# Kernel tuning notes

Hardware: AMD Instinct MI355X
Metric: run time of the kernel (lower is better)

The kernel has to match this reference:

```python
import jax, jax.numpy as jnp
import numpy as np

EPS = 1e-5

def _bn(x):
    # BatchNorm (training-mode batch stats, gamma=1, beta=0) over batch+spatial axes
    axes = (0,) + tuple(range(2, x.ndim))
    m = x.mean(axis=axes, keepdims=True)
    v = x.var(axis=axes, keepdims=True)
    return (x - m) / jnp.sqrt(v + EPS)

def _knn(x, k):
    # x: [B, C, N] -> idx [B, N, K] of k nearest neighbors (largest of negative sq dist)
    xt = jnp.swapaxes(x, 1, 2)                      # [B, N, C]
    inner = -2.0 * jnp.einsum('bnc,bmc->bnm', xt, xt)
    xx = jnp.sum(x * x, axis=1)                     # [B, N]
    pdist = -xx[:, :, None] - inner - xx[:, None, :]  # [B, N, N] (negative sq dist)
    return jax.lax.top_k(pdist, k)[1]

def _get_neighbors(x, k):
    # x: [B, C, N] -> edge features [B, 2C, N, K] = concat(neighbor - center, center)
    idx = _knn(x, k)                                # [B, N, K]
    xt = jnp.swapaxes(x, 1, 2)                      # [B, N, C]
    nb = jax.vmap(lambda pts, i: pts[i])(xt, idx)   # [B, N, K, C]
    center = jnp.broadcast_to(xt[:, :, None, :], nb.shape)
    feat = jnp.concatenate([nb - center, center], axis=-1)  # [B, N, K, 2C]
    return jnp.transpose(feat, (0, 3, 1, 2))        # [B, 2C, N, K]

def _sa_layer(x, Wq, Wk, Wt, bt):
    # Faithful SALayerSingleHead: note original computes x_v but never uses it,
    # and uses x @ attention; we match that math exactly. x: [B, C, N]
    xq = jnp.einsum('qc,bcn->bnq', Wq, x)           # [B, N, C/4]
    xk = jnp.einsum('qc,bcn->bqn', Wk, x)           # [B, C/4, N]
    energy = jnp.einsum('bnq,bqm->bnm', xq, xk)     # [B, N, N]
    attn = jax.nn.softmax(energy, axis=-1)
    attn = attn / (1e-6 + attn.sum(axis=1, keepdims=True))
    xr = jnp.einsum('bcn,bnm->bcm', x, attn)        # [B, C, N]
    xr = jax.nn.relu(_bn(jnp.einsum('oc,bcn->bon', Wt, x - xr) + bt[None, :, None]))
    return x + xr

def setup_inputs() -> dict:
    key = jax.random.key(0)
    ks = jax.random.split(key, 12)
    B, N, K = 8, 2048, 32
    s = 0.02
    inp = {
        'x': jax.random.normal(ks[0], (B, 3, N), dtype=jnp.float32),
        'We1': jax.random.normal(ks[1], (64, 6), dtype=jnp.float32) * s,
        'be1': jnp.zeros((64,), jnp.float32),
        'We2': jax.random.normal(ks[2], (64, 128), dtype=jnp.float32) * s,
        'be2': jnp.zeros((64,), jnp.float32),
        'Wq': jax.random.normal(ks[3], (4, 32, 128), dtype=jnp.float32) * s,
        'Wk': jax.random.normal(ks[4], (4, 32, 128), dtype=jnp.float32) * s,
        'Wt': jax.random.normal(ks[5], (4, 128, 128), dtype=jnp.float32) * s,
        'bt': jnp.zeros((4, 128), jnp.float32),
        'Wf': jax.random.normal(ks[6], (1024, 512), dtype=jnp.float32) * s,
        'bf': jnp.zeros((1024,), jnp.float32),
        'Wc1': jax.random.normal(ks[7], (512, 1536), dtype=jnp.float32) * s,
        'bc1': jnp.zeros((512,), jnp.float32),
        'Wc2': jax.random.normal(ks[8], (256, 512), dtype=jnp.float32) * s,
        'bc2': jnp.zeros((256,), jnp.float32),
        'Wc3': jax.random.normal(ks[9], (13, 256), dtype=jnp.float32) * s,
        'bc3': jnp.zeros((13,), jnp.float32),
        'k': K,
    }
    return inp

def reference(x, We1, be1, We2, be2, Wq, Wk, Wt, bt, Wf, bf, Wc1, bc1, Wc2, bc2, Wc3, bc3, k):
    # EdgeConv block 1: xyz -> 64
    e1 = jnp.einsum('oc,bcnk->bonk', We1, _get_neighbors(x, k)) + be1[None, :, None, None]
    f1 = jax.nn.relu(_bn(e1)).max(axis=-1)          # [B, 64, N]
    # EdgeConv block 2: 64 -> 64
    e2 = jnp.einsum('oc,bcnk->bonk', We2, _get_neighbors(f1, k)) + be2[None, :, None, None]
    f2 = jax.nn.relu(_bn(e2)).max(axis=-1)          # [B, 64, N]
    feat = jnp.concatenate([f1, f2], axis=1)        # [B, 128, N]
    # 4 stacked single-head SA layers (PCT offset attention)
    xs = feat
    outs = []
    for i in range(4):
        xs = _sa_layer(xs, Wq[i], Wk[i], Wt[i], bt[i])
        outs.append(xs)
    cat = jnp.concatenate(outs, axis=1)             # [B, 512, N]
    fuse = jax.nn.relu(_bn(jnp.einsum('oc,bcn->bon', Wf, cat) + bf[None, :, None]))  # [B,1024,N]
    g = fuse.max(axis=-1)                           # [B, 1024]
    gl = jnp.broadcast_to(g[:, :, None], (g.shape[0], g.shape[1], cat.shape[2]))
    h = jnp.concatenate([gl, cat], axis=1)          # [B, 1536, N]
    h = jax.nn.relu(_bn(jnp.einsum('oc,bcn->bon', Wc1, h) + bc1[None, :, None]))
    h = jax.nn.relu(_bn(jnp.einsum('oc,bcn->bon', Wc2, h) + bc2[None, :, None]))
    out = jnp.einsum('oc,bcn->bon', Wc3, h) + bc3[None, :, None]  # [B, 13, N]
    return out
```

## Files before the change

### kernel.cpp

```cpp
#include <hip/hip_runtime.h>
#include <math.h>

#define DEV static __device__ __forceinline__

namespace {

constexpr int B = 8;
constexpr int N = 2048;
constexpr int KNN = 32;
constexpr float BNEPS = 1e-5f;

DEV unsigned f2key(float f) {
  unsigned u = __float_as_uint(f);
  return (u & 0x80000000u) ? ~u : (u | 0x80000000u);
}

DEV void atomicMaxFloat(float* addr, float val) {
  if (val >= 0.0f) atomicMax((int*)addr, __float_as_int(val));
  else atomicMin((unsigned int*)addr, (unsigned int)__float_as_int(val));
}

struct SelScratch {
  unsigned hist[256];
  int ss[257];
  int bin;
  int cnt;
};

template <int NK>
DEV unsigned long long radix_select32(const unsigned long long (&keys)[NK], SelScratch& s) {
  const int t = threadIdx.x;
  const int lane = t & 63, wave = t >> 6;
  unsigned long long prefix = 0; unsigned long long T = 0;
  int needed = KNN;
  bool done = false;
  for (int level = 0; level < 8 && !done; ++level) {
    int shift = 56 - 8 * level;
    s.hist[t] = 0;
    __syncthreads();
    unsigned long long maskhi = level ? (~0ull << (64 - 8 * level)) : 0ull;
    #pragma unroll
    for (int j = 0; j < NK; ++j) {
      if ((keys[j] & maskhi) == prefix)
        atomicAdd(&s.hist[(unsigned)(keys[j] >> shift) & 255u], 1u);
    }
    __syncthreads();
    if (wave == 0) {
      unsigned h0 = s.hist[4 * lane], h1 = s.hist[4 * lane + 1], h2 = s.hist[4 * lane + 2], h3 = s.hist[4 * lane + 3];
      unsigned s3 = h3, s2 = h2 + s3, s1 = h1 + s2, s0 = h0 + s1;
      unsigned suf = s0;
      #pragma unroll
      for (int off = 1; off < 64; off <<= 1) {
        unsigned v = __shfl_down(suf, off);
        if (lane + off < 64) suf += v;
      }
      unsigned above = suf - s0;
      s.ss[4 * lane] = (int)(s0 + above); s.ss[4 * lane + 1] = (int)(s1 + above);
      s.ss[4 * lane + 2] = (int)(s2 + above); s.ss[4 * lane + 3] = (int)(s3 + above);
      if (lane == 63) s.ss[256] = 0;
    }
    __syncthreads();
    if (s.ss[t] >= needed && s.ss[t + 1] < needed) s.bin = t;
    __syncthreads();
    int bin = s.bin;
    int hc = (int)s.hist[bin];
    needed -= s.ss[bin + 1];
    prefix |= ((unsigned long long)(unsigned)bin) << shift;
    if (needed == hc) { T = prefix; done = true; }
    __syncthreads();
  }
  return T;
}

template <int NK>
DEV void collect32(const unsigned long long (&keys)[NK], unsigned long long T, SelScratch& s,
                   int* __restrict__ out) {
  if (threadIdx.x == 0) s.cnt = 0;
  __syncthreads();
  #pragma unroll
  for (int j = 0; j < NK; ++j) {
    if (keys[j] >= T) {
      int pos = atomicAdd(&s.cnt, 1);
      out[pos] = (int)~(unsigned)keys[j];
    }
  }
  __syncthreads();
}

__global__ __launch_bounds__(256) void knn1_kernel(const float* __restrict__ x, int* __restrict__ idx) {
  __shared__ SelScratch s;
  __shared__ double cc[3];
  int bn = blockIdx.x, b = bn >> 11, n = bn & (N - 1);
  int t = threadIdx.x;
  const float* xb = x + (size_t)b * 3 * N;
  if (t < 3) cc[t] = (double)xb[(size_t)t * N + n];
  __syncthreads();
  double cx = cc[0], cy = cc[1], cz = cc[2];
  unsigned long long keys[8];
  #pragma unroll
  for (int j = 0; j < 8; ++j) {
    int m = t + 256 * j;
    double dx = (double)xb[m] - cx, dy = (double)xb[N + m] - cy, dz = (double)xb[2 * N + m] - cz;
    double pd = -(dx * dx + dy * dy + dz * dz);
    keys[j] = ((unsigned long long)f2key((float)pd) << 32) | (unsigned)~m;
  }
  __syncthreads();
  unsigned long long T = radix_select32(keys, s);
  collect32(keys, T, s, idx + (size_t)bn * KNN);
}

__global__ __launch_bounds__(256) void edge1_kernel(const float* __restrict__ x, const int* __restrict__ idx,
    const float* __restrict__ We1, const float* __restrict__ be1,
    float* __restrict__ emax, double* __restrict__ epart) {
  __shared__ float Ws[6][65];
  __shared__ float fs[6][33];
  __shared__ float es[64][33];
  __shared__ int  is[KNN];
  int bn = blockIdx.x, b = bn >> 11, n = bn & (N - 1);
  int t = threadIdx.x;
  if (t < KNN) is[t] = idx[(size_t)bn * KNN + t];
  for (int e = t; e < 64 * 6; e += 256) Ws[e % 6][e / 6] = We1[e];
  __syncthreads();
  const float* xb = x + (size_t)b * 3 * N;
  for (int e = t; e < 6 * KNN; e += 256) {
    int c = e >> 5, k = e & 31;
    int m = is[k];
    fs[c][k] = (c < 3) ? (xb[(size_t)c * N + m] - xb[(size_t)c * N + n]) : xb[(size_t)(c - 3) * N + n];
  }
  __syncthreads();
  int k = t & 31, orow = t >> 5;
  float acc[8];
  #pragma unroll
  for (int j = 0; j < 8; ++j) acc[j] = 0.0f;
  #pragma unroll
  for (int c = 0; c < 6; ++c) {
    float fv = fs[c][k];
    #pragma unroll
    for (int j = 0; j < 8; ++j) acc[j] = __fadd_rn(acc[j], __fmul_rn(Ws[c][orow * 8 + j], fv));
  }
  #pragma unroll
  for (int j = 0; j < 8; ++j) es[orow * 8 + j][k] = __fadd_rn(acc[j], be1[orow * 8 + j]);
  __syncthreads();
  if (t < 64) {
    double sum = 0, s2 = 0; float mx = -3.402823466e38f;
    #pragma unroll 8
    for (int kk = 0; kk < KNN; ++kk) {
      float v = es[t][kk]; double dv = (double)v;
      sum += dv; s2 = fma(dv, dv, s2); mx = fmaxf(mx, v);
    }
    emax[((size_t)b * 64 + t) * N + n] = mx;
    epart[(size_t)bn * 128 + t] = sum;
    epart[(size_t)bn * 128 + 64 + t] = s2;
  }
}

__global__ __launch_bounds__(256) void edge_stats_kernel(const double* __restrict__ epart, float* __restrict__ ems) {
  __shared__ double r1[256], r2[256];
  int o = blockIdx.x, t = threadIdx.x;
  double s = 0, s2 = 0;
  for (int i = t; i < B * N; i += 256) { s += epart[(size_t)i * 128 + o]; s2 += epart[(size_t)i * 128 + 64 + o]; }
  r1[t] = s; r2[t] = s2; __syncthreads();
  for (int st = 128; st > 0; st >>= 1) { if (t < st) { r1[t] += r1[t + st]; r2[t] += r2[t + st]; } __syncthreads(); }
  if (t == 0) {
    double cnt = (double)(B * N * KNN);
    double m = r1[0] / cnt, v = r2[0] / cnt - m * m;
    ems[o] = (float)m; ems[64 + o] = (float)v;
  }
}

__global__ __launch_bounds__(256) void edge_finish_kernel(const float* __restrict__ emax, const float* __restrict__ ems,
                                                          float* __restrict__ f) {
  size_t i = (size_t)blockIdx.x * 256 + threadIdx.x;
  int c = (int)((i >> 11) & 63);
  float sd = sqrtf(ems[64 + c] + BNEPS);
  float v = (emax[i] - ems[c]) / sd;
  f[i] = v > 0.f ? v : 0.f;
}

__global__ __launch_bounds__(256) void transpose_f1_kernel(const float* __restrict__ f1, float* __restrict__ f1t) {
  size_t i = (size_t)blockIdx.x * 256 + threadIdx.x;
  int n = (int)(i & (N - 1)); int c = (int)((i >> 11) & 63); int b = (int)(i >> 17);
  f1t[((size_t)b * N + n) * 64 + c] = f1[i];
}

__global__ __launch_bounds__(256) void xx2_kernel(const float* __restrict__ f1, double* __restrict__ xx2) {
  int i = blockIdx.x * 256 + threadIdx.x;
  int b = i >> 11, n = i & (N - 1);
  const float* p = f1 + (size_t)b * 64 * N + n;
  double s = 0;
  #pragma unroll 16
  for (int c = 0; c < 64; ++c) { double v = (double)p[(size_t)c * N]; s = fma(v, v, s); }
  xx2[i] = s;
}

__global__ __launch_bounds__(256) void knn2_kernel(const float* __restrict__ f1, const float* __restrict__ f1t,
                                                   const double* __restrict__ xx2, int* __restrict__ idx) {
  __shared__ SelScratch s;
  __shared__ double ctr[4][64];
  int bx = blockIdx.x, b = bx >> 9, n0 = (bx & 511) * 4;
  int t = threadIdx.x;
  { int i = t >> 6, c = t & 63; ctr[i][c] = (double)f1t[((size_t)b * N + n0 + i) * 64 + c]; }
  __syncthreads();
  const float* fb = f1 + (size_t)b * 64 * N;
  const double* xxb = xx2 + (size_t)b * N;
  double xxn0 = xxb[n0], xxn1 = xxb[n0 + 1], xxn2 = xxb[n0 + 2], xxn3 = xxb[n0 + 3];
  unsigned long long keys[4][8];
  #pragma unroll 1
  for (int j = 0; j < 8; ++j) {
    int m = t + 256 * j;
    double a0 = 0, a1 = 0, a2 = 0, a3 = 0;
    #pragma unroll 8
    for (int c = 0; c < 64; ++c) {
      double v = (double)fb[(size_t)c * N + m];
      a0 = fma(v, ctr[0][c], a0); a1 = fma(v, ctr[1][c], a1);
      a2 = fma(v, ctr[2][c], a2); a3 = fma(v, ctr[3][c], a3);
    }
    double xxm = xxb[m];
    double p0 = -xxn0 + 2.0 * a0 - xxm, p1 = -xxn1 + 2.0 * a1 - xxm;
    double p2 = -xxn2 + 2.0 * a2 - xxm, p3 = -xxn3 + 2.0 * a3 - xxm;
    unsigned long long lo = (unsigned)~m;
    keys[0][j] = ((unsigned long long)f2key((float)p0) << 32) | lo;
    keys[1][j] = ((unsigned long long)f2key((float)p1) << 32) | lo;
    keys[2][j] = ((unsigned long long)f2key((float)p2) << 32) | lo;
    keys[3][j] = ((unsigned long long)f2key((float)p3) << 32) | lo;
  }
  __syncthreads();
  #pragma unroll 1
  for (int i = 0; i < 4; ++i) {
    unsigned long long T = radix_select32(keys[i], s);
    collect32(keys[i], T, s, idx + ((size_t)b * N + n0 + i) * KNN);
  }
}

__global__ __launch_bounds__(256) void edge2_kernel(const float* __restrict__ f1t, const int* __restrict__ idx,
    const float* __restrict__ We2, const float* __restrict__ be2,
    float* __restrict__ emax, double* __restrict__ epart) {
  __shared__ float smem[8448];
  __shared__ int is[4][32];
  float (*Ws)[65] = (float(*)[65])smem;
  float* fsb = smem + 2080;
  int bx = blockIdx.x;
  int b = bx >> 9, n0 = (bx & 511) * 4;
  int t = threadIdx.x;
  if (t < 128) is[t >> 5][t & 31] = idx[((size_t)b * N + n0 + (t >> 5)) * KNN + (t & 31)];
  int k = t & 31, p = (t >> 5) & 3, oh = t >> 7;
  float acc[32];
  #pragma unroll
  for (int j = 0; j < 32; ++j) acc[j] = 0.f;
  const float* fbt = f1t + (size_t)b * N * 64;
  for (int cc = 0; cc < 4; ++cc) {
    int c0 = cc * 32;
    __syncthreads();
    for (int e = t; e < 2048; e += 256) Ws[e & 31][e >> 5] = We2[(size_t)(e >> 5) * 128 + c0 + (e & 31)];
    for (int e = t; e < 4096; e += 256) {
      int c = e & 31, kk = (e >> 5) & 31, pp = e >> 10;
      int m = is[pp][kk];
      int cg = c0 + c;
      float v = (cg < 64) ? (fbt[(size_t)m * 64 + cg] - fbt[(size_t)(n0 + pp) * 64 + cg])
                          : fbt[(size_t)(n0 + pp) * 64 + (cg - 64)];
      fsb[(pp * 32 + c) * 33 + kk] = v;
    }
    __syncthreads();
    #pragma unroll 4
    for (int c = 0; c < 32; ++c) {
      float fv = fsb[(p * 32 + c) * 33 + k];
      #pragma unroll
      for (int j = 0; j < 32; ++j) acc[j] = fmaf(Ws[c][oh * 32 + j], fv, acc[j]);
    }
  }
  __syncthreads();
  #pragma unroll
  for (int j = 0; j < 32; ++j) smem[((p * 64 + oh * 32 + j)) * 33 + k] = acc[j] + be2[oh * 32 + j];
  __syncthreads();
  {
    int pp = t >> 6, o = t & 63;
    const float* ep = smem + (pp * 64 + o) * 33;
    double sum = 0, s2 = 0; float mx = -3.402823466e38f;
    #pragma unroll 8
    for (int kk = 0; kk < KNN; ++kk) {
      float v = ep[kk]; double dv = (double)v;
      sum += dv; s2 = fma(dv, dv, s2); mx = fmaxf(mx, v);
    }
    int n = n0 + pp;
    emax[((size_t)b * 64 + o) * N + n] = mx;
    epart[((size_t)b * N + n) * 128 + o] = sum;
    epart[((size_t)b * N + n) * 128 + 64 + o] = s2;
  }
}

__global__ __launch_bounds__(256) void concat_feat_kernel(const float* __restrict__ f1, const float* __restrict__ f2,
                                                          float* __restrict__ feat) {
  size_t i = (size_t)blockIdx.x * 256 + threadIdx.x;
  int n = (int)(i & (N - 1)); int c = (int)((i >> 11) & 127); int b = (int)(i >> 18);
  feat[i] = (c < 64) ? f1[((size_t)b * 64 + c) * N + n] : f2[((size_t)b * 64 + (c - 64)) * N + n];
}

__global__ __launch_bounds__(256) void sa_qk_kernel(const float* __restrict__ xs, int xs_bstride, int xs_coff,
    const float* __restrict__ Wq, const float* __restrict__ Wk,
    float* __restrict__ xq, float* __restrict__ xk) {
  __shared__ __align__(16) float Ws[32][68];
  __shared__ __align__(16) float vs[32][68];
  int bx = blockIdx.x, b = bx >> 5, n0 = (bx & 31) * 64;
  int t = threadIdx.x;
  int tc = t >> 4, tm = t & 15;
  float acc[4][4];
  #pragma unroll
  for (int i = 0; i < 4; ++i)
    #pragma unroll
    for (int j = 0; j < 4; ++j) acc[i][j] = 0.f;
  for (int cc = 0; cc < 4; ++cc) {
    int c0 = cc * 32;
    __syncthreads();
    for (int e = t; e < 512; e += 256) {
      int o = e >> 3, cq = e & 7;
      float4 w4 = (o < 32) ? *(const float4*)&Wq[o * 128 + c0 + cq * 4]
                           : *(const float4*)&Wk[(o - 32) * 128 + c0 + cq * 4];
      Ws[cq * 4 + 0][o] = w4.x; Ws[cq * 4 + 1][o] = w4.y; Ws[cq * 4 + 2][o] = w4.z; Ws[cq * 4 + 3][o] = w4.w;
    }
    for (int e = t; e < 512; e += 256) {
      int c = e >> 4, nq = e & 15;
      *(float4*)&vs[c][nq * 4] =
          *(const float4*)&xs[(size_t)b * xs_bstride + (size_t)(xs_coff + c0 + c) * N + n0 + nq * 4];
    }
    __syncthreads();
    #pragma unroll 4
    for (int c = 0; c < 32; ++c) {
      float4 w4 = *(const float4*)&Ws[c][tc * 4];
      float4 v4 = *(const float4*)&vs[c][tm * 4];
      float wv[4] = {w4.x, w4.y, w4.z, w4.w};
      float vv[4] = {v4.x, v4.y, v4.z, v4.w};
      #pragma unroll
      for (int i = 0; i < 4; ++i)
        #pragma unroll
        for (int j = 0; j < 4; ++j) acc[i][j] = fmaf(wv[i], vv[j], acc[i][j]);
    }
  }
  #pragma unroll
  for (int i = 0; i < 4; ++i) {
    int o2 = tc * 4 + i;
    if (o2 < 32) {
      #pragma unroll
      for (int j = 0; j < 4; ++j) {
        int n = n0 + tm * 4 + j;
        xq[((size_t)b * N + n) * 32 + o2] = acc[i][j];
      }
    } else {
      float4 o4 = make_float4(acc[i][0], acc[i][1], acc[i][2], acc[i][3]);
      *(float4*)&xk[((size_t)b * 32 + (o2 - 32)) * N + n0 + tm * 4] = o4;
    }
  }
}

__global__ __launch_bounds__(256) void sa_rowstats_kernel(const float* __restrict__ xq, const float* __restrict__ xk,
    float* __restrict__ rowmax, float* __restrict__ rowsum) {
  __shared__ float qs[16][33];
  __shared__ float wred[4][16][2];
  int bx = blockIdx.x;
  int b = bx >> 7, n0 = (bx & 127) * 16;
  int t = threadIdx.x;
  for (int e = t; e < 16 * 32; e += 256) qs[e >> 5][e & 31] = xq[((size_t)b * N + n0 + (e >> 5)) * 32 + (e & 31)];
  __syncthreads();
  float rm[16], rs[16];
  #pragma unroll
  for (int r = 0; r < 16; ++r) { rm[r] = -3.402823466e38f; rs[r] = 0.f; }
  const float* xkb = xk + (size_t)b * 32 * N;
  for (int m = t; m < N; m += 256) {
    float kv[32];
    #pragma unroll
    for (int q = 0; q < 32; ++q) kv[q] = xkb[(size_t)q * N + m];
    #pragma unroll 4
    for (int r = 0; r < 16; ++r) {
      float e = 0;
      #pragma unroll
      for (int q = 0; q < 32; ++q) e = fmaf(qs[r][q], kv[q], e);
      if (e > rm[r]) { rs[r] = rs[r] * __expf(rm[r] - e) + 1.0f; rm[r] = e; }
      else rs[r] += __expf(e - rm[r]);
    }
  }
  int lane = t & 63, w = t >> 6;
  #pragma unroll 1
  for (int r = 0; r < 16; ++r) {
    float m1 = rm[r], s1 = rs[r];
    #pragma unroll
    for (int off = 32; off > 0; off >>= 1) {
      float m2 = __shfl_xor(m1, off), s2 = __shfl_xor(s1, off);
      float mm = fmaxf(m1, m2);
      s1 = s1 * __expf(m1 - mm) + s2 * __expf(m2 - mm);
      m1 = mm;
    }
    if (lane == 0) { wred[w][r][0] = m1; wred[w][r][1] = s1; }
  }
  __syncthreads();
  if (t < 16) {
    float M = wred[0][t][0], S = wred[0][t][1];
    #pragma unroll
    for (int w2 = 1; w2 < 4; ++w2) {
      float m2 = wred[w2][t][0], s2 = wred[w2][t][1];
      float mm = fmaxf(M, m2);
      S = S * __expf(M - mm) + s2 * __expf(m2 - mm);
      M = mm;
    }
    rowmax[(size_t)b * N + n0 + t] = M;
    rowsum[(size_t)b * N + n0 + t] = S;
  }
}

__global__ __launch_bounds__(256) void sa_attny_kernel(const float* __restrict__ xs, int xs_bstride, int xs_coff,
    const float* __restrict__ xq, const float* __restrict__ xk,
    const float* __restrict__ rowmax, const float* __restrict__ rowsum,
    float* __restrict__ Yp, float* __restrict__ cspart) {
  __shared__ __align__(16) float qs[64][36];
  __shared__ float rmv[64], rsv[64];
  __shared__ __align__(16) float Ps[64][68];
  __shared__ __align__(16) float vs[64][132];
  __shared__ float csr[4][64];
  int bx = blockIdx.x;
  int g = bx & 3, m0 = ((bx >> 2) & 31) * 64, b = bx >> 7;
  int t = threadIdx.x;
  int tc = t >> 4, tm = t & 15;
  int tmm = t & 63, tns = t >> 6;
  float kreg[32];
  #pragma unroll
  for (int q = 0; q < 32; ++q) kreg[q] = xk[((size_t)b * 32 + q) * N + m0 + tmm];
  float acc[2][4][4];
  #pragma unroll
  for (int h = 0; h < 2; ++h)
    #pragma unroll
    for (int i = 0; i < 4; ++i)
      #pragma unroll
      for (int j = 0; j < 4; ++j) acc[h][i][j] = 0.f;
  float cs = 0.f;
  const float* xsb = xs + (size_t)b * xs_bstride + (size_t)xs_coff * N;
  for (int nt = g * 8; nt < g * 8 + 8; ++nt) {
    int n0 = nt * 64;
    __syncthreads();
    for (int e = t; e < 512; e += 256) {
      int nn = e >> 3, qq = e & 7;
      *(float4*)&qs[nn][qq * 4] = *(const float4*)&xq[((size_t)b * N + n0 + nn) * 32 + qq * 4];
    }
    if (t < 64) { rmv[t] = rowmax[(size_t)b * N + n0 + t]; rsv[t] = 1.0f / rowsum[(size_t)b * N + n0 + t]; }
    for (int e = t; e < 128 * 64; e += 256) { int c = e >> 6, nn = e & 63; vs[nn][c] = xsb[(size_t)c * N + n0 + nn]; }
    __syncthreads();
    float cp = 0.f;
    #pragma unroll 1
    for (int jj = 0; jj < 16; ++jj) {
      int nn = tns * 16 + jj;
      float ea = 0, eb = 0, ec = 0, ed = 0;
      #pragma unroll
      for (int q4 = 0; q4 < 8; ++q4) {
        float4 qv = *(const float4*)&qs[nn][q4 * 4];
        ea = fmaf(qv.x, kreg[4 * q4 + 0], ea);
        eb = fmaf(qv.y, kreg[4 * q4 + 1], eb);
        ec = fmaf(qv.z, kreg[4 * q4 + 2], ec);
        ed = fmaf(qv.w, kreg[4 * q4 + 3], ed);
      }
      float e2 = (ea + eb) + (ec + ed);
      float p = __expf(e2 - rmv[nn]) * rsv[nn];
      Ps[nn][tmm] = p; cp += p;
    }
    csr[tns][tmm] = cp;
    __syncthreads();
    if (t < 64) cs += csr[0][t] + csr[1][t] + csr[2][t] + csr[3][t];
    #pragma unroll 2
    for (int nn = 0; nn < 64; ++nn) {
      float4 pa = *(const float4*)&Ps[nn][tm * 4];
      float4 x0 = *(const float4*)&vs[nn][tc * 4];
      float4 x1 = *(const float4*)&vs[nn][64 + tc * 4];
      float pvv[4] = {pa.x, pa.y, pa.z, pa.w};
      float xv0[4] = {x0.x, x0.y, x0.z, x0.w};
      float xv1[4] = {x1.x, x1.y, x1.z, x1.w};
      #pragma unroll
      for (int i = 0; i < 4; ++i)
        #pragma unroll
        for (int jm = 0; jm < 4; ++jm) {
          acc[0][i][jm] = fmaf(xv0[i], pvv[jm], acc[0][i][jm]);
          acc[1][i][jm] = fmaf(xv1[i], pvv[jm], acc[1][i][jm]);
        }
    }
  }
  #pragma unroll
  for (int h = 0; h < 2; ++h)
    #pragma unroll
    for (int i = 0; i < 4; ++i) {
      float4 o4 = make_float4(acc[h][i][0], acc[h][i][1], acc[h][i][2], acc[h][i][3]);
      *(float4*)&Yp[(((size_t)g * B + b) * 128 + h * 64 + tc * 4 + i) * N + m0 + tm * 4] = o4;
    }
  if (t < 64) cspart[((size_t)g * B + b) * N + m0 + t] = cs;
}

__global__ __launch_bounds__(256) void sa_wt_kernel(const float* __restrict__ xs, int xs_bstride, int xs_coff,
    const float* __restrict__ Yp, const float* __restrict__ cspart,
    const float* __restrict__ Wt, const float* __restrict__ bt,
    float* __restrict__ tpre) {
  __shared__ __align__(16) float Ws[32][132];
  __shared__ __align__(16) float vs[32][68];
  __shared__ __align__(16) float inv[64];
  int bx = blockIdx.x, b = bx >> 5, n0 = (bx & 31) * 64;
  int t = threadIdx.x;
  if (t < 64) {
    float s = 0;
    #pragma unroll
    for (int g = 0; g < 4; ++g) s += cspart[((size_t)g * B + b) * N + n0 + t];
    inv[t] = 1.0f / (1e-6f + s);
  }
  int tc = t >> 4, tm = t & 15;
  float acc[8][4];
  #pragma unroll
  for (int jc = 0; jc < 8; ++jc)
    #pragma unroll
    for (int jm = 0; jm < 4; ++jm) acc[jc][jm] = 0.f;
  for (int cc = 0; cc < 4; ++cc) {
    int c0 = cc * 32;
    __syncthreads();
    for (int e = t; e < 1024; e += 256) {
      int o = e >> 3, cq = e & 7;
      float4 w4 = *(const float4*)&Wt[o * 128 + c0 + cq * 4];
      Ws[cq * 4 + 0][o] = w4.x; Ws[cq * 4 + 1][o] = w4.y; Ws[cq * 4 + 2][o] = w4.z; Ws[cq * 4 + 3][o] = w4.w;
    }
    for (int e = t; e < 512; e += 256) {
      int c = e >> 4, nq = e & 15;
      float4 xv = *(const float4*)&xs[(size_t)b * xs_bstride + (size_t)(xs_coff + c0 + c) * N + n0 + nq * 4];
      float4 ys = make_float4(0.f, 0.f, 0.f, 0.f);
      #pragma unroll
      for (int g = 0; g < 4; ++g) {
        float4 yv = *(const float4*)&Yp[(((size_t)g * B + b) * 128 + c0 + c) * N + n0 + nq * 4];
        ys.x += yv.x; ys.y += yv.y; ys.z += yv.z; ys.w += yv.w;
      }
      float4 iv = *(const float4*)&inv[nq * 4];
      float4 r = make_float4(xv.x - ys.x * iv.x, xv.y - ys.y * iv.y, xv.z - ys.z * iv.z, xv.w - ys.w * iv.w);
      *(float4*)&vs[c][nq * 4] = r;
    }
    __syncthreads();
    #pragma unroll 4
    for (int c = 0; c < 32; ++c) {
      float4 w0 = *(const float4*)&Ws[c][tc * 4];
      float4 w1 = *(const float4*)&Ws[c][tc * 4 + 64];
      float4 v4 = *(const float4*)&vs[c][tm * 4];
      float wv[8] = {w0.x, w0.y, w0.z, w0.w, w1.x, w1.y, w1.z, w1.w};
      float vv[4] = {v4.x, v4.y, v4.z, v4.w};
      #pragma unroll
      for (int jc = 0; jc < 8; ++jc)
        #pragma unroll
        for (int jm = 0; jm < 4; ++jm) acc[jc][jm] = fmaf(wv[jc], vv[jm], acc[jc][jm]);
    }
  }
  #pragma unroll
  for (int jc = 0; jc < 8; ++jc) {
    int o2 = tc * 4 + (jc & 3) + (jc >> 2) * 64;
    float bias = bt[o2];
    float4 o4 = make_float4(acc[jc][0] + bias, acc[jc][1] + bias, acc[jc][2] + bias, acc[jc][3] + bias);
    *(float4*)&tpre[((size_t)b * 128 + o2) * N + n0 + tm * 4] = o4;
  }
}

__global__ __launch_bounds__(256) void chanstats_kernel(const float* __restrict__ x, float* __restrict__ ms, int C) {
  __shared__ double r1[256], r2[256];
  int c = blockIdx.x, t = threadIdx.x;
  double s = 0, s2 = 0;
  for (int i = t; i < B * N; i += 256) {
    int b = i >> 11, n = i & (N - 1);
    double v = (double)x[((size_t)b * C + c) * N + n];
    s += v; s2 = fma(v, v, s2);
  }
  r1[t] = s; r2[t] = s2; __syncthreads();
  for (int st = 128; st > 0; st >>= 1) { if (t < st) { r1[t] += r1[t + st]; r2[t] += r2[t + st]; } __syncthreads(); }
  if (t == 0) {
    double cnt = (double)(B * N);
    double m = r1[0] / cnt, v = r2[0] / cnt - m * m;
    ms[c] = (float)m; ms[C + c] = (float)v;
  }
}

__global__ __launch_bounds__(256) void sa_out_kernel(const float* __restrict__ tpre, const float* __restrict__ ms,
    const float* __restrict__ xs, int xs_bstride, int xs_coff, float* __restrict__ cat, int lay) {
  size_t i = (size_t)blockIdx.x * 256 + threadIdx.x;
  int n = (int)(i & (N - 1)); int c = (int)((i >> 11) & 127); int b = (int)(i >> 18);
  float sd = sqrtf(ms[128 + c] + BNEPS);
  float v = (tpre[i] - ms[c]) / sd;
  v = v > 0.f ? v : 0.f;
  float xv = xs[(size_t)b * xs_bstride + (size_t)(xs_coff + c) * N + n];
  cat[((size_t)b * 512 + lay * 128 + c) * N + n] = xv + v;
}

__global__ __launch_bounds__(256) void fuse_kernel(const float* __restrict__ cat, const float* __restrict__ Wf,
    const float* __restrict__ bf, float* __restrict__ fps, float* __restrict__ fps2, float* __restrict__ premax) {
  __shared__ __align__(16) float smem[8320];
  float (*Ws)[132] = (float(*)[132])smem;
  float (*vs)[68] = (float(*)[68])(smem + 4224);
  int bx = blockIdx.x;
  int b = bx >> 8, o0 = ((bx >> 5) & 7) * 128, n0 = (bx & 31) * 64;
  int part = b * 32 + (bx & 31);
  int t = threadIdx.x, tc = t >> 4, tm = t & 15;
  float acc[8][4];
  #pragma unroll
  for (int jc = 0; jc < 8; ++jc)
    #pragma unroll
    for (int jm = 0; jm < 4; ++jm) acc[jc][jm] = 0.f;
  for (int cc = 0; cc < 16; ++cc) {
    int c0 = cc * 32;
    __syncthreads();
    for (int e = t; e < 1024; e += 256) {
      int o = e >> 3, cq = e & 7;
      float4 w4 = *(const float4*)&Wf[(size_t)(o0 + o) * 512 + c0 + cq * 4];
      Ws[cq * 4 + 0][o] = w4.x; Ws[cq * 4 + 1][o] = w4.y; Ws[cq * 4 + 2][o] = w4.z; Ws[cq * 4 + 3][o] = w4.w;
    }
    for (int e = t; e < 512; e += 256) {
      int c = e >> 4, nq = e & 15;
      *(float4*)&vs[c][nq * 4] = *(const float4*)&cat[((size_t)b * 512 + c0 + c) * N + n0 + nq * 4];
    }
    __syncthreads();
    #pragma unroll 4
    for (int c = 0; c < 32; ++c) {
      float4 w0 = *(const float4*)&Ws[c][tc * 4];
      float4 w1 = *(const float4*)&Ws[c][tc * 4 + 64];
      float4 v4 = *(const float4*)&vs[c][tm * 4];
      float wv[8] = {w0.x, w0.y, w0.z, w0.w, w1.x, w1.y, w1.z, w1.w};
      float vv[4] = {v4.x, v4.y, v4.z, v4.w};
      #pragma unroll
      for (int jc = 0; jc < 8; ++jc)
        #pragma unroll
        for (int jm = 0; jm < 4; ++jm) acc[jc][jm] = fmaf(wv[jc], vv[jm], acc[jc][jm]);
    }
  }
  __syncthreads();
  #pragma unroll
  for (int jc = 0; jc < 8; ++jc) {
    int o = tc * 4 + (jc & 3) + (jc >> 2) * 64;
    float bias = bf[o0 + o];
    #pragma unroll
    for (int jm = 0; jm < 4; ++jm) smem[o * 65 + tm * 4 + jm] = acc[jc][jm] + bias;
  }
  __syncthreads();
  if (t < 128) {
    double s = 0, s2 = 0; float mx = -3.402823466e38f;
    const float* dp = smem + t * 65;
    #pragma unroll 8
    for (int nn = 0; nn < 64; ++nn) {
      float v = dp[nn]; double dv = (double)v;
      s += dv; s2 = fma(dv, dv, s2); mx = fmaxf(mx, v);
    }
    fps[(size_t)(o0 + t) * 256 + part] = (float)s;
    fps2[(size_t)(o0 + t) * 256 + part] = (float)s2;
    atomicMaxFloat(&premax[(size_t)b * 1024 + o0 + t], mx);
  }
}

__global__ __launch_bounds__(256) void fuse_stats_kernel(const float* __restrict__ fps, const float* __restrict__ fps2,
                                                         float* __restrict__ ms) {
  __shared__ double r1[256], r2[256];
  int o = blockIdx.x, t = threadIdx.x;
  r1[t] = (double)fps[(size_t)o * 256 + t];
  r2[t] = (double)fps2[(size_t)o * 256 + t];
  __syncthreads();
  for (int st = 128; st > 0; st >>= 1) { if (t < st) { r1[t] += r1[t + st]; r2[t] += r2[t + st]; } __syncthreads(); }
  if (t == 0) {
    double cnt = (double)(B * N);
    double m = r1[0] / cnt, v = r2[0] / cnt - m * m;
    ms[o] = (float)m; ms[1024 + o] = (float)v;
  }
}

__global__ void g_kernel(const float* __restrict__ premax, const float* __restrict__ ms, float* __restrict__ g) {
  int i = blockIdx.x * 256 + threadIdx.x;
  int o = i & 1023;
  float sd = sqrtf(ms[1024 + o] + BNEPS);
  float v = (premax[i] - ms[o]) / sd;
  g[i] = v > 0.f ? v : 0.f;
}

__global__ __launch_bounds__(256) void gproj_kernel(const float* __restrict__ Wc1, const float* __restrict__ g,
                                                    float* __restrict__ gproj) {
  int i = blockIdx.x * 256 + threadIdx.x;
  int b = i >> 9, o = i & 511;
  const float* gb = g + (size_t)b * 1024;
  const float* wr = Wc1 + (size_t)o * 1536;
  float s = 0;
  #pragma unroll 8
  for (int c = 0; c < 1024; ++c) s = fmaf(wr[c], gb[c], s);
  gproj[i] = s;
}

__global__ __launch_bounds__(256) void mlp_gemm_kernel(const float* __restrict__ in, int Cin,
    const float* __restrict__ W, int wstride, int wcoff,
    const float* __restrict__ bias, const float* __restrict__ extra, int Cout,
    float* __restrict__ out) {
  __shared__ __align__(16) float Ws[32][132];
  __shared__ __align__(16) float vs[32][68];
  int otiles = Cout >> 7;
  int bx = blockIdx.x;
  int b = bx / (otiles * 32); int rem = bx % (otiles * 32);
  int o0 = (rem >> 5) * 128, n0 = (rem & 31) * 64;
  int t = threadIdx.x, tc = t >> 4, tm = t & 15;
  float acc[8][4];
  #pragma unroll
  for (int jc = 0; jc < 8; ++jc)
    #pragma unroll
    for (int jm = 0; jm < 4; ++jm) acc[jc][jm] = 0.f;
  for (int c0 = 0; c0 < Cin; c0 += 32) {
    __syncthreads();
    for (int e = t; e < 1024; e += 256) {
      int o = e >> 3, cq = e & 7;
      float4 w4 = *(const float4*)&W[(size_t)(o0 + o) * wstride + wcoff + c0 + cq * 4];
      Ws[cq * 4 + 0][o] = w4.x; Ws[cq * 4 + 1][o] = w4.y; Ws[cq * 4 + 2][o] = w4.z; Ws[cq * 4 + 3][o] = w4.w;
    }
    for (int e = t; e < 512; e += 256) {
      int c = e >> 4, nq = e & 15;
      *(float4*)&vs[c][nq * 4] = *(const float4*)&in[((size_t)b * Cin + c0 + c) * N + n0 + nq * 4];
    }
    __syncthreads();
    #pragma unroll 4
    for (int c = 0; c < 32; ++c) {
      float4 w0 = *(const float4*)&Ws[c][tc * 4];
      float4 w1 = *(const float4*)&Ws[c][tc * 4 + 64];
      float4 v4 = *(const float4*)&vs[c][tm * 4];
      float wv[8] = {w0.x, w0.y, w0.z, w0.w, w1.x, w1.y, w1.z, w1.w};
      float vv[4] = {v4.x, v4.y, v4.z, v4.w};
      #pragma unroll
      for (int jc = 0; jc < 8; ++jc)
        #pragma unroll
        for (int jm = 0; jm < 4; ++jm) acc[jc][jm] = fmaf(wv[jc], vv[jm], acc[jc][jm]);
    }
  }
  #pragma unroll
  for (int jc = 0; jc < 8; ++jc) {
    int o2 = o0 + tc * 4 + (jc & 3) + (jc >> 2) * 64;
    float add = bias[o2] + (extra ? extra[(size_t)b * Cout + o2] : 0.f);
    float4 o4 = make_float4(acc[jc][0] + add, acc[jc][1] + add, acc[jc][2] + add, acc[jc][3] + add);
    *(float4*)&out[((size_t)b * Cout + o2) * N + n0 + tm * 4] = o4;
  }
}

__global__ void bnrelu_inplace_kernel(float* __restrict__ x, const float* __restrict__ ms, int C) {
  size_t i = (size_t)blockIdx.x * 256 + threadIdx.x;
  int c = (int)((i >> 11) & (C - 1));
  float sd = sqrtf(ms[C + c] + BNEPS);
  float v = (x[i] - ms[c]) / sd;
  x[i] = v > 0.f ? v : 0.f;
}

__global__ __launch_bounds__(256) void wc3_kernel(const float* __restrict__ h, const float* __restrict__ Wc3,
                                                  const float* __restrict__ bc3, float* __restrict__ out) {
  __shared__ float Ws[13][257];
  int bx = blockIdx.x;
  int b = bx >> 3, n0 = (bx & 7) * 256;
  int t = threadIdx.x;
  for (int e = t; e < 13 * 256; e += 256) { int o = e >> 8, c = e & 255; Ws[o][c] = Wc3[o * 256 + c]; }
  __syncthreads();
  float s[13];
  #pragma unroll
  for (int o = 0; o < 13; ++o) s[o] = 0.f;
  const float* hb = h + (size_t)b * 256 * N + n0 + t;
  #pragma unroll 4
  for (int c = 0; c < 256; ++c) {
    float hv = hb[(size_t)c * N];
    #pragma unroll
    for (int o = 0; o < 13; ++o) s[o] = fmaf(Ws[o][c], hv, s[o]);
  }
  #pragma unroll
  for (int o = 0; o < 13; ++o) out[((size_t)b * 13 + o) * N + n0 + t] = s[o] + bc3[o];
}

__global__ void init_kernel(float* __restrict__ premax) {
  int i = blockIdx.x * 256 + threadIdx.x;
  if (i < 8192) premax[i] = -3.402823466e38f;
}

}

extern "C" void kernel_launch(void* const* d_in, const int* in_sizes, int n_in,
                              void* d_out, int out_size, void* d_ws, size_t ws_size,
                              hipStream_t stream) {
  const float* x   = (const float*)d_in[0];
  const float* We1 = (const float*)d_in[1];
  const float* be1 = (const float*)d_in[2];
  const float* We2 = (const float*)d_in[3];
  const float* be2 = (const float*)d_in[4];
  const float* Wq  = (const float*)d_in[5];
  const float* Wk  = (const float*)d_in[6];
  const float* Wt  = (const float*)d_in[7];
  const float* bt  = (const float*)d_in[8];
  const float* Wf  = (const float*)d_in[9];
  const float* bf  = (const float*)d_in[10];
  const float* Wc1 = (const float*)d_in[11];
  const float* bc1 = (const float*)d_in[12];
  const float* Wc2 = (const float*)d_in[13];
  const float* bc2 = (const float*)d_in[14];
  const float* Wc3 = (const float*)d_in[15];
  const float* bc3 = (const float*)d_in[16];
  float* out = (float*)d_out;

  char* w = (char*)d_ws;
  size_t off = 0;
  auto take = [&](size_t nbytes) { void* p = w + off; off += (nbytes + 255) & ~(size_t)255; return p; };
  int*    idx1   = (int*)   take((size_t)B * N * KNN * 4);
  int*    idx2   = (int*)   take((size_t)B * N * KNN * 4);
  float*  f1     = (float*) take((size_t)B * 64 * N * 4);
  float*  f2     = (float*) take((size_t)B * 64 * N * 4);
  float*  f1t    = (float*) take((size_t)B * N * 64 * 4);
  double* xx2d   = (double*)take((size_t)B * N * 8);
  double* epart  = (double*)take((size_t)B * N * 128 * 8);
  float*  emax   = (float*) take((size_t)B * 64 * N * 4);
  float*  ems    = (float*) take(128 * 4);
  float*  feat   = (float*) take((size_t)B * 128 * N * 4);
  float*  cat    = (float*) take((size_t)B * 512 * N * 4);
  float*  xq     = (float*) take((size_t)B * N * 32 * 4);
  float*  xk     = (float*) take((size_t)B * 32 * N * 4);
  float*  rowmax = (float*) take((size_t)B * N * 4);
  float*  rowsum = (float*) take((size_t)B * N * 4);
  float*  ubuf   = (float*) take((size_t)B * 256 * N * 4);
  float*  tpre   = ubuf + (size_t)B * 128 * N;
  float*  pre2   = ubuf;
  float*  bnstats= (float*) take(2048 * 4);
  float*  fps    = (float*) take((size_t)1024 * 256 * 4);
  float*  fps2   = (float*) take((size_t)1024 * 256 * 4);
  float*  premax = (float*) take((size_t)B * 1024 * 4);
  float*  gbuf   = (float*) take((size_t)B * 1024 * 4);
  float*  gproj  = (float*) take((size_t)B * 512 * 4);
  float*  pre1   = (float*) take((size_t)B * 512 * N * 4);
  float*  Yp     = pre1;
  float*  cspart = fps;
  (void)ws_size; (void)in_sizes; (void)n_in; (void)out_size;

  init_kernel<<<32, 256, 0, stream>>>(premax);

  knn1_kernel<<<B * N, 256, 0, stream>>>(x, idx1);
  edge1_kernel<<<B * N, 256, 0, stream>>>(x, idx1, We1, be1, emax, epart);
  edge_stats_kernel<<<64, 256, 0, stream>>>(epart, ems);
  edge_finish_kernel<<<B * 64 * N / 256, 256, 0, stream>>>(emax, ems, f1);

  transpose_f1_kernel<<<B * 64 * N / 256, 256, 0, stream>>>(f1, f1t);
  xx2_kernel<<<B * N / 256, 256, 0, stream>>>(f1, xx2d);
  knn2_kernel<<<B * N / 4, 256, 0, stream>>>(f1, f1t, xx2d, idx2);
  edge2_kernel<<<B * 512, 256, 0, stream>>>(f1t, idx2, We2, be2, emax, epart);
  edge_stats_kernel<<<64, 256, 0, stream>>>(epart, ems);
  edge_finish_kernel<<<B * 64 * N / 256, 256, 0, stream>>>(emax, ems, f2);
  concat_feat_kernel<<<B * 128 * N / 256, 256, 0, stream>>>(f1, f2, feat);

  for (int lay = 0; lay < 4; ++lay) {
    const float* xs = lay ? cat : feat;
    int bstride = lay ? 512 * N : 128 * N;
    int coff = lay ? (lay - 1) * 128 : 0;
    sa_qk_kernel<<<B * 32, 256, 0, stream>>>(xs, bstride, coff, Wq + lay * 32 * 128, Wk + lay * 32 * 128, xq, xk);
    sa_rowstats_kernel<<<B * 128, 256, 0, stream>>>(xq, xk, rowmax, rowsum);
    sa_attny_kernel<<<B * 32 * 4, 256, 0, stream>>>(xs, bstride, coff, xq, xk, rowmax, rowsum, Yp, cspart);
    sa_wt_kernel<<<B * 32, 256, 0, stream>>>(xs, bstride, coff, Yp, cspart, Wt + lay * 128 * 128, bt + lay * 128, tpre);
    chanstats_kernel<<<128, 256, 0, stream>>>(tpre, bnstats, 128);
    sa_out_kernel<<<B * 128 * N / 256, 256, 0, stream>>>(tpre, bnstats, xs, bstride, coff, cat, lay);
  }

  fuse_kernel<<<B * 8 * 32, 256, 0, stream>>>(cat, Wf, bf, fps, fps2, premax);
  fuse_stats_kernel<<<1024, 256, 0, stream>>>(fps, fps2, bnstats);
  g_kernel<<<B * 1024 / 256, 256, 0, stream>>>(premax, bnstats, gbuf);

  gproj_kernel<<<B * 512 / 256, 256, 0, stream>>>(Wc1, gbuf, gproj);
  mlp_gemm_kernel<<<B * 4 * 32, 256, 0, stream>>>(cat, 512, Wc1, 1536, 1024, bc1, gproj, 512, pre1);
  chanstats_kernel<<<512, 256, 0, stream>>>(pre1, bnstats, 512);
  bnrelu_inplace_kernel<<<B * 512 * N / 256, 256, 0, stream>>>(pre1, bnstats, 512);

  mlp_gemm_kernel<<<B * 2 * 32, 256, 0, stream>>>(pre1, 512, Wc2, 512, 0, bc2, nullptr, 256, pre2);
  chanstats_kernel<<<256, 256, 0, stream>>>(pre2, bnstats, 256);
  bnrelu_inplace_kernel<<<B * 256 * N / 256, 256, 0, stream>>>(pre2, bnstats, 256);

  wc3_kernel<<<B * 8, 256, 0, stream>>>(pre2, Wc3, bc3, out);
}
```

Before: 2.582 ms.

## Retile edge2 GEMM, swizzle attention V tile, fuse f1 transpose into finish

Three unrelated changes. The f1 transpose kernel is folded into edge_finish, which now also writes the point-major copy. edge2 switches from one neighbor per thread with 32 outputs to a 4-output by 8-neighbor register tile fed by float4 shared-memory loads, with padding adjusted for alignment. The attention-times-V loop stores its V tile with an XOR swizzle to avoid LDS bank conflicts and un-permutes values in registers. Together these cut shared-memory traffic and one launch, at the cost of more index arithmetic and a strided scattered store in edge_finish.

```diff
diff --git a/kernel.cpp b/kernel.cpp
--- a/kernel.cpp
+++ b/kernel.cpp
@@ -169,18 +169,17 @@
 }
 
 __global__ __launch_bounds__(256) void edge_finish_kernel(const float* __restrict__ emax, const float* __restrict__ ems,
-                                                          float* __restrict__ f) {
+                                                          float* __restrict__ f, float* __restrict__ ft) {
   size_t i = (size_t)blockIdx.x * 256 + threadIdx.x;
   int c = (int)((i >> 11) & 63);
   float sd = sqrtf(ems[64 + c] + BNEPS);
   float v = (emax[i] - ems[c]) / sd;
-  f[i] = v > 0.f ? v : 0.f;
-}
-
-__global__ __launch_bounds__(256) void transpose_f1_kernel(const float* __restrict__ f1, float* __restrict__ f1t) {
-  size_t i = (size_t)blockIdx.x * 256 + threadIdx.x;
-  int n = (int)(i & (N - 1)); int c = (int)((i >> 11) & 63); int b = (int)(i >> 17);
-  f1t[((size_t)b * N + n) * 64 + c] = f1[i];
+  v = v > 0.f ? v : 0.f;
+  f[i] = v;
+  if (ft) {
+    int n = (int)(i & (N - 1)); int b = (int)(i >> 17);
+    ft[((size_t)b * N + n) * 64 + c] = v;
+  }
 }
 
 __global__ __launch_bounds__(256) void xx2_kernel(const float* __restrict__ f1, double* __restrict__ xx2) {
@@ -235,50 +234,64 @@
 __global__ __launch_bounds__(256) void edge2_kernel(const float* __restrict__ f1t, const int* __restrict__ idx,
     const float* __restrict__ We2, const float* __restrict__ be2,
     float* __restrict__ emax, double* __restrict__ epart) {
-  __shared__ float smem[8448];
+  __shared__ __align__(16) float smem[8448];
   __shared__ int is[4][32];
-  float (*Ws)[65] = (float(*)[65])smem;
-  float* fsb = smem + 2080;
+  float* Wsb = smem;
+  float* fsb = smem + 2176;
   int bx = blockIdx.x;
   int b = bx >> 9, n0 = (bx & 511) * 4;
   int t = threadIdx.x;
   if (t < 128) is[t >> 5][t & 31] = idx[((size_t)b * N + n0 + (t >> 5)) * KNN + (t & 31)];
-  int k = t & 31, p = (t >> 5) & 3, oh = t >> 7;
-  float acc[32];
-  #pragma unroll
-  for (int j = 0; j < 32; ++j) acc[j] = 0.f;
+  int o4 = t & 15, kq = (t >> 4) & 3, p = t >> 6;
+  float acc[4][8];
+  #pragma unroll
+  for (int i = 0; i < 4; ++i)
+    #pragma unroll
+    for (int j = 0; j < 8; ++j) acc[i][j] = 0.f;
   const float* fbt = f1t + (size_t)b * N * 64;
   for (int cc = 0; cc < 4; ++cc) {
     int c0 = cc * 32;
     __syncthreads();
-    for (int e = t; e < 2048; e += 256) Ws[e & 31][e >> 5] = We2[(size_t)(e >> 5) * 128 + c0 + (e & 31)];
+    for (int e = t; e < 2048; e += 256) { int o = e >> 5, c = e & 31; Wsb[c * 68 + o] = We2[(size_t)o * 128 + c0 + c]; }
     for (int e = t; e < 4096; e += 256) {
       int c = e & 31, kk = (e >> 5) & 31, pp = e >> 10;
       int m = is[pp][kk];
       int cg = c0 + c;
       float v = (cg < 64) ? (fbt[(size_t)m * 64 + cg] - fbt[(size_t)(n0 + pp) * 64 + cg])
                           : fbt[(size_t)(n0 + pp) * 64 + (cg - 64)];
-      fsb[(pp * 32 + c) * 33 + kk] = v;
+      fsb[(pp * 32 + c) * 36 + kk] = v;
     }
     __syncthreads();
     #pragma unroll 4
     for (int c = 0; c < 32; ++c) {
-      float fv = fsb[(p * 32 + c) * 33 + k];
-      #pragma unroll
-      for (int j = 0; j < 32; ++j) acc[j] = fmaf(Ws[c][oh * 32 + j], fv, acc[j]);
-    }
-  }
-  __syncthreads();
-  #pragma unroll
-  for (int j = 0; j < 32; ++j) smem[((p * 64 + oh * 32 + j)) * 33 + k] = acc[j] + be2[oh * 32 + j];
+      float4 w4 = *(const float4*)&Wsb[c * 68 + o4 * 4];
+      float4 fa = *(const float4*)&fsb[(p * 32 + c) * 36 + kq * 8];
+      float4 fb = *(const float4*)&fsb[(p * 32 + c) * 36 + kq * 8 + 4];
+      float wv[4]; *(float4*)wv = w4;
+      float fv[8]; *(float4*)fv = fa; *(float4*)(fv + 4) = fb;
+      #pragma unroll
+      for (int i = 0; i < 4; ++i)
+        #pragma unroll
+        for (int j = 0; j < 8; ++j) acc[i][j] = fmaf(wv[i], fv[j], acc[i][j]);
+    }
+  }
+  __syncthreads();
+  {
+    float bv[4]; *(float4*)bv = *(const float4*)&be2[o4 * 4];
+    #pragma unroll
+    for (int j = 0; j < 8; ++j) {
+      int k = kq * 8 + j;
+      float4 v4 = make_float4(acc[0][j] + bv[0], acc[1][j] + bv[1], acc[2][j] + bv[2], acc[3][j] + bv[3]);
+      *(float4*)&smem[k * 264 + p * 64 + o4 * 4] = v4;
+    }
+  }
   __syncthreads();
   {
     int pp = t >> 6, o = t & 63;
-    const float* ep = smem + (pp * 64 + o) * 33;
     double sum = 0, s2 = 0; float mx = -3.402823466e38f;
     #pragma unroll 8
     for (int kk = 0; kk < KNN; ++kk) {
-      float v = ep[kk]; double dv = (double)v;
+      float v = smem[kk * 264 + pp * 64 + o]; double dv = (double)v;
       sum += dv; s2 = fma(dv, dv, s2); mx = fmaxf(mx, v);
     }
     int n = n0 + pp;
@@ -439,7 +452,11 @@
       *(float4*)&qs[nn][qq * 4] = *(const float4*)&xq[((size_t)b * N + n0 + nn) * 32 + qq * 4];
     }
     if (t < 64) { rmv[t] = rowmax[(size_t)b * N + n0 + t]; rsv[t] = 1.0f / rowsum[(size_t)b * N + n0 + t]; }
-    for (int e = t; e < 128 * 64; e += 256) { int c = e >> 6, nn = e & 63; vs[nn][c] = xsb[(size_t)c * N + n0 + nn]; }
+    for (int e = t; e < 128 * 64; e += 256) {
+      int c = e >> 6, nn = e & 63;
+      int M = (nn & 3) | (((nn >> 3) & 7) << 2);
+      vs[nn][c ^ M] = xsb[(size_t)c * N + n0 + nn];
+    }
     __syncthreads();
     float cp = 0.f;
     #pragma unroll 1
@@ -461,21 +478,30 @@
     csr[tns][tmm] = cp;
     __syncthreads();
     if (t < 64) cs += csr[0][t] + csr[1][t] + csr[2][t] + csr[3][t];
-    #pragma unroll 2
-    for (int nn = 0; nn < 64; ++nn) {
-      float4 pa = *(const float4*)&Ps[nn][tm * 4];
-      float4 x0 = *(const float4*)&vs[nn][tc * 4];
-      float4 x1 = *(const float4*)&vs[nn][64 + tc * 4];
-      float pvv[4] = {pa.x, pa.y, pa.z, pa.w};
-      float xv0[4] = {x0.x, x0.y, x0.z, x0.w};
-      float xv1[4] = {x1.x, x1.y, x1.z, x1.w};
-      #pragma unroll
-      for (int i = 0; i < 4; ++i)
+    #pragma unroll 1
+    for (int nn8 = 0; nn8 < 8; ++nn8) {
+      int s2x = nn8 << 2;
+      int b0 = (tc * 4) ^ s2x;
+      #pragma unroll
+      for (int kk = 0; kk < 8; ++kk) {
+        int nn = nn8 * 8 + kk;
+        const int k = kk & 3;
+        float4 pa = *(const float4*)&Ps[nn][tm * 4];
+        float4 q0 = *(const float4*)&vs[nn][b0];
+        float4 q1 = *(const float4*)&vs[nn][64 + b0];
+        float pv[4]; *(float4*)pv = pa;
+        float xr0[4]; *(float4*)xr0 = q0;
+        float xr1[4]; *(float4*)xr1 = q1;
+        float xv0[4] = {xr0[0 ^ k], xr0[1 ^ k], xr0[2 ^ k], xr0[3 ^ k]};
+        float xv1[4] = {xr1[0 ^ k], xr1[1 ^ k], xr1[2 ^ k], xr1[3 ^ k]};
         #pragma unroll
-        for (int jm = 0; jm < 4; ++jm) {
-          acc[0][i][jm] = fmaf(xv0[i], pvv[jm], acc[0][i][jm]);
-          acc[1][i][jm] = fmaf(xv1[i], pvv[jm], acc[1][i][jm]);
-        }
+        for (int i = 0; i < 4; ++i)
+          #pragma unroll
+          for (int jm = 0; jm < 4; ++jm) {
+            acc[0][i][jm] = fmaf(xv0[i], pv[jm], acc[0][i][jm]);
+            acc[1][i][jm] = fmaf(xv1[i], pv[jm], acc[1][i][jm]);
+          }
+      }
     }
   }
   #pragma unroll
@@ -826,14 +852,13 @@
   knn1_kernel<<<B * N, 256, 0, stream>>>(x, idx1);
   edge1_kernel<<<B * N, 256, 0, stream>>>(x, idx1, We1, be1, emax, epart);
   edge_stats_kernel<<<64, 256, 0, stream>>>(epart, ems);
-  edge_finish_kernel<<<B * 64 * N / 256, 256, 0, stream>>>(emax, ems, f1);
-
-  transpose_f1_kernel<<<B * 64 * N / 256, 256, 0, stream>>>(f1, f1t);
+  edge_finish_kernel<<<B * 64 * N / 256, 256, 0, stream>>>(emax, ems, f1, f1t);
+
   xx2_kernel<<<B * N / 256, 256, 0, stream>>>(f1, xx2d);
   knn2_kernel<<<B * N / 4, 256, 0, stream>>>(f1, f1t, xx2d, idx2);
   edge2_kernel<<<B * 512, 256, 0, stream>>>(f1t, idx2, We2, be2, emax, epart);
   edge_stats_kernel<<<64, 256, 0, stream>>>(epart, ems);
-  edge_finish_kernel<<<B * 64 * N / 256, 256, 0, stream>>>(emax, ems, f2);
+  edge_finish_kernel<<<B * 64 * N / 256, 256, 0, stream>>>(emax, ems, f2, nullptr);
   concat_feat_kernel<<<B * 128 * N / 256, 256, 0, stream>>>(f1, f2, feat);
 
   for (int lay = 0; lay < 4; ++lay) {
```

After: 2.448 ms. 5.2% less time.
